# Optimization experiments

Hardware: AMD Instinct MI355X
Metric: run time of the kernel (lower is better)

Reference implementation:

```python
import jax, jax.numpy as jnp
import numpy as np

NUM_DAYOFWEEK, NUM_TIME, NUM_MONTH, NUM_DAY = 7, 24, 12, 31
NUM_DESTINATION = 100000
NUM_FACTOR = 128
NUM_DIM = NUM_FACTOR // 4  # 32
N = 1048576


def setup_inputs() -> dict:
    key = jax.random.key(0)
    ks = jax.random.split(key, 10)
    std = 0.1
    return {
        "dayofweek": jax.random.randint(ks[0], (N,), 0, NUM_DAYOFWEEK),
        "time": jax.random.randint(ks[1], (N,), 0, NUM_TIME),
        "month": jax.random.randint(ks[2], (N,), 0, NUM_MONTH),
        "day": jax.random.randint(ks[3], (N,), 0, NUM_DAY),
        "destination": jax.random.randint(ks[4], (N,), 0, NUM_DESTINATION),
        "W_dayofweek": std * jax.random.normal(ks[5], (NUM_DAYOFWEEK, NUM_DIM), dtype=jnp.float32),
        "W_time": std * jax.random.normal(ks[6], (NUM_TIME, NUM_DIM), dtype=jnp.float32),
        "W_month": std * jax.random.normal(ks[7], (NUM_MONTH, NUM_DIM), dtype=jnp.float32),
        "W_day": std * jax.random.normal(ks[8], (NUM_DAY, NUM_DIM), dtype=jnp.float32),
        "W_item": std * jax.random.normal(ks[9], (NUM_DESTINATION, NUM_FACTOR), dtype=jnp.float32),
    }


def reference(dayofweek, time, month, day, destination,
              W_dayofweek, W_time, W_month, W_day, W_item) -> jnp.ndarray:
    # Gather per-feature embeddings and concat into user vector [N, num_factor]
    user = jnp.concatenate([
        W_dayofweek[dayofweek],  # [N, 32]
        W_time[time],            # [N, 32]
        W_month[month],          # [N, 32]
        W_day[day],              # [N, 32]
    ], axis=-1)
    item = W_item[destination]   # [N, 128]
    # Original: diagonal(mm(user, item.T)) == rowwise dot product; compute it directly.
    return jnp.sum(user * item, axis=-1)  # [N]
```

## Files before the change

### kernel.cpp

```cpp
#include <hip/hip_runtime.h>


constexpr int NDIM = 32;
constexpr int TS   = 36;
constexpr int R_DOW = 7, R_TIM = 24, R_MON = 12, R_DAY = 31;
constexpr int B_DOW = 0;
constexpr int B_TIM = B_DOW + R_DOW * TS;
constexpr int B_MON = B_TIM + R_TIM * TS;
constexpr int B_DAY = B_MON + R_MON * TS;
constexpr int TAB_TOT = B_DAY + R_DAY * TS;

constexpr int NB   = 32;
constexpr int DDIV = 3125;
constexpr int NBLK = 512;
constexpr int SPB  = 2048;
constexpr int IPT  = SPB / 256;

typedef unsigned long long u64;

__device__ __forceinline__ void load_tab(float* tab, const float* Wdow, const float* Wtim,
                                         const float* Wmon, const float* Wday) {
    const int t = threadIdx.x;
    for (int i = t; i < R_DOW * NDIM; i += 256) tab[B_DOW + (i >> 5) * TS + (i & 31)] = Wdow[i];
    for (int i = t; i < R_TIM * NDIM; i += 256) tab[B_TIM + (i >> 5) * TS + (i & 31)] = Wtim[i];
    for (int i = t; i < R_MON * NDIM; i += 256) tab[B_MON + (i >> 5) * TS + (i & 31)] = Wmon[i];
    for (int i = t; i < R_DAY * NDIM; i += 256) tab[B_DAY + (i >> 5) * TS + (i & 31)] = Wday[i];
}

__global__ __launch_bounds__(256, 2)
void bin_kernel(const int* __restrict__ dow, const int* __restrict__ tim,
                const int* __restrict__ mon, const int* __restrict__ day,
                const int* __restrict__ dest,
                int* __restrict__ cntG, int* __restrict__ lbaseG,
                u64* __restrict__ payload, unsigned short* __restrict__ invl, int n)
{
    __shared__ u64 stage[SPB];
    __shared__ unsigned short ist[SPB];
    __shared__ int hist[NB], lbase[NB], cursor[NB];

    const int t = threadIdx.x, b = blockIdx.x;
    const int g0 = b * SPB;
    const int rem = n - g0;
    const int len = rem < SPB ? rem : SPB;

    int dreg[IPT], pkreg[IPT];
#pragma unroll
    for (int i = 0; i < IPT; i++) {
        const int k = i * 256 + t;
        if (k < len) {
            const int idx = g0 + k;
            dreg[i]  = dest[idx];
            pkreg[i] = dow[idx] | (tim[idx] << 3) | (mon[idx] << 8) | (day[idx] << 12);
        } else { dreg[i] = -1; pkreg[i] = 0; }
    }
    if (t < NB) hist[t] = 0;
    __syncthreads();
#pragma unroll
    for (int i = 0; i < IPT; i++)
        if (dreg[i] >= 0) atomicAdd(&hist[dreg[i] / DDIV], 1);
    __syncthreads();
    if (t == 0) {
        int run = 0;
        for (int q = 0; q < NB; q++) { lbase[q] = run; run += hist[q]; }
    }
    __syncthreads();
    if (t < NB) { cursor[t] = lbase[t]; cntG[b * NB + t] = hist[t]; lbaseG[b * NB + t] = lbase[t]; }
    __syncthreads();
#pragma unroll
    for (int i = 0; i < IPT; i++) {
        const int k = i * 256 + t;
        if (k < len) {
            const int ds = dreg[i];
            const int j  = atomicAdd(&cursor[ds / DDIV], 1);
            stage[j] = (u64)(unsigned)(g0 + k)
                     | ((u64)(unsigned)ds       << 20)
                     | ((u64)(unsigned)pkreg[i] << 37);
            ist[k] = (unsigned short)j;
        }
    }
    __syncthreads();
#pragma unroll
    for (int i = 0; i < IPT; i++) {
        const int k = i * 256 + t;
        if (k < len) {
            payload[g0 + k] = stage[k];
            invl[g0 + k]    = ist[k];
        }
    }
}

__global__ __launch_bounds__(256, 8)
void mf_main_kernel(const u64* __restrict__ payload,
                    const float* __restrict__ Wdow, const float* __restrict__ Wtim,
                    const float* __restrict__ Wmon, const float* __restrict__ Wday,
                    const float* __restrict__ Witem,
                    const int* __restrict__ cntG, const int* __restrict__ lbaseG,
                    float* __restrict__ res)
{
    __shared__ float tab[TAB_TOT];
    load_tab(tab, Wdow, Wtim, Wmon, Wday);
    __syncthreads();

    const int tid = threadIdx.x;
    const int sub = tid & 63;
    const int wv  = tid >> 6;
    const int g   = sub >> 3;
    const int l8  = sub & 7;
    const int col = l8 * 4;
    const int tb[4] = {B_DOW, B_TIM, B_MON, B_DAY};
    const int sh[4] = {37, 40, 45, 49};
    const int mk[4] = {7, 31, 15, 31};

    const int x = blockIdx.x & 7;
    const int s = blockIdx.x >> 3;

    for (int p = 0; p < 4; p++) {
        const int q  = x + 8 * p;
        const int L  = cntG[s * NB + q];
        const int st = s * SPB + lbaseG[s * NB + q];

        for (int i = wv * 16; i < L; i += 64) {
            const int i0 = i + g, i1 = i + 8 + g;
            const bool v0 = i0 < L, v1 = i1 < L;

            const u64 p0 = v0 ? payload[st + i0] : 0ull;
            const u64 p1 = v1 ? payload[st + i1] : 0ull;

            const int d0 = (int)((p0 >> 20) & 0x1FFFFull);
            const int d1 = (int)((p1 >> 20) & 0x1FFFFull);

            const float* r0 = Witem + (long)d0 * 128 + col;
            const float* r1 = Witem + (long)d1 * 128 + col;

            float4 it0[4], it1[4], us0[4], us1[4];
#pragma unroll
            for (int j = 0; j < 4; j++) it0[j] = *reinterpret_cast<const float4*>(r0 + j * NDIM);
#pragma unroll
            for (int j = 0; j < 4; j++) it1[j] = *reinterpret_cast<const float4*>(r1 + j * NDIM);
#pragma unroll
            for (int j = 0; j < 4; j++) {
                const int idx = (int)((p0 >> sh[j]) & (u64)mk[j]);
                us0[j] = *reinterpret_cast<const float4*>(&tab[tb[j] + idx * TS + col]);
            }
#pragma unroll
            for (int j = 0; j < 4; j++) {
                const int idx = (int)((p1 >> sh[j]) & (u64)mk[j]);
                us1[j] = *reinterpret_cast<const float4*>(&tab[tb[j] + idx * TS + col]);
            }

            float a0 = 0.f, a1 = 0.f;
#pragma unroll
            for (int j = 0; j < 4; j++) {
                a0 += it0[j].x * us0[j].x + it0[j].y * us0[j].y
                    + it0[j].z * us0[j].z + it0[j].w * us0[j].w;
                a1 += it1[j].x * us1[j].x + it1[j].y * us1[j].y
                    + it1[j].z * us1[j].z + it1[j].w * us1[j].w;
            }

            a0 += __shfl_xor(a0, 1);  a1 += __shfl_xor(a1, 1);
            a0 += __shfl_xor(a0, 2);  a1 += __shfl_xor(a1, 2);
            a0 += __shfl_xor(a0, 4);  a1 += __shfl_xor(a1, 4);

            if (l8 == 0) {
                if (v0) res[st + i0] = a0;
                if (v1) res[st + i1] = a1;
            }
        }
    }
}

__global__ __launch_bounds__(256, 2)
void unperm_kernel(const float* __restrict__ res, const unsigned short* __restrict__ invl,
                   float* __restrict__ out, int n)
{
    __shared__ float r[SPB];
    const int t = threadIdx.x, b = blockIdx.x;
    const int g0 = b * SPB;
    const int rem = n - g0;
    const int len = rem < SPB ? rem : SPB;
#pragma unroll
    for (int i = 0; i < IPT; i++) {
        const int k = i * 256 + t;
        if (k < len) r[k] = res[g0 + k];
    }
    __syncthreads();
#pragma unroll
    for (int i = 0; i < IPT; i++) {
        const int k = i * 256 + t;
        if (k < len) out[g0 + k] = r[invl[g0 + k]];
    }
}

__global__ __launch_bounds__(256, 8)
void mf_dot_kernel(const int* __restrict__ dow, const int* __restrict__ tim,
                   const int* __restrict__ mon, const int* __restrict__ day,
                   const int* __restrict__ dest,
                   const float* __restrict__ Wdow, const float* __restrict__ Wtim,
                   const float* __restrict__ Wmon, const float* __restrict__ Wday,
                   const float* __restrict__ Witem,
                   float* __restrict__ out, int n_samples)
{
    __shared__ float tab[TAB_TOT];
    load_tab(tab, Wdow, Wtim, Wmon, Wday);
    __syncthreads();
    const int tid = threadIdx.x;
    const int lane = tid & 63, sub = lane & 31, wave = tid >> 6, half = lane >> 5;
    const int t = sub >> 3, dofs = (sub & 7) * 4;
    const int* idxp  = (t == 0) ? dow   : (t == 1) ? tim   : (t == 2) ? mon   : day;
    const int  tbase = (t == 0) ? B_DOW : (t == 1) ? B_TIM : (t == 2) ? B_MON : B_DAY;
    long n = (long)blockIdx.x * 8 + wave * 2 + half;
    const long stride = (long)gridDim.x * 8;
    for (; n < n_samples; n += stride) {
        const int idx = idxp[n];
        const int ds  = dest[n];
        const float4 u  = *reinterpret_cast<const float4*>(&tab[tbase + idx * TS + dofs]);
        const float4 it = *reinterpret_cast<const float4*>(&Witem[(long)ds * 128 + sub * 4]);
        float r = u.x * it.x + u.y * it.y + u.z * it.z + u.w * it.w;
        r += __shfl_xor(r, 16); r += __shfl_xor(r, 8); r += __shfl_xor(r, 4);
        r += __shfl_xor(r, 2);  r += __shfl_xor(r, 1);
        if (sub == 0) out[n] = r;
    }
}

extern "C" void kernel_launch(void* const* d_in, const int* in_sizes, int n_in,
                              void* d_out, int out_size, void* d_ws, size_t ws_size,
                              hipStream_t stream)
{
    const int*   dow   = (const int*)d_in[0];
    const int*   tim   = (const int*)d_in[1];
    const int*   mon   = (const int*)d_in[2];
    const int*   day   = (const int*)d_in[3];
    const int*   dest  = (const int*)d_in[4];
    const float* Wdow  = (const float*)d_in[5];
    const float* Wtim  = (const float*)d_in[6];
    const float* Wmon  = (const float*)d_in[7];
    const float* Wday  = (const float*)d_in[8];
    const float* Witem = (const float*)d_in[9];
    float* out = (float*)d_out;

    const int n = in_sizes[0];
    const int cap = NBLK * SPB;

    const size_t off_payload = 128 * 1024;
    const size_t off_invl    = off_payload + (size_t)cap * 8;
    const size_t off_res     = off_invl + (size_t)cap * 2;
    const size_t need        = off_res + (size_t)cap * 4;

    if ((size_t)ws_size < need || n > cap) {
        hipLaunchKernelGGL(mf_dot_kernel, dim3(2048), dim3(256), 0, stream,
                           dow, tim, mon, day, dest,
                           Wdow, Wtim, Wmon, Wday, Witem, out, n);
        return;
    }

    int* cntG    = (int*)d_ws;
    int* lbaseG  = (int*)((char*)d_ws + 64 * 1024);
    u64* payload = (u64*)((char*)d_ws + off_payload);
    unsigned short* invl = (unsigned short*)((char*)d_ws + off_invl);
    float* res           = (float*)((char*)d_ws + off_res);

    hipLaunchKernelGGL(bin_kernel, dim3(NBLK), dim3(256), 0, stream,
                       dow, tim, mon, day, dest, cntG, lbaseG, payload, invl, n);
    hipLaunchKernelGGL(mf_main_kernel, dim3(NBLK * 8), dim3(256), 0, stream,
                       payload, Wdow, Wtim, Wmon, Wday, Witem, cntG, lbaseG, res);
    hipLaunchKernelGGL(unperm_kernel, dim3(NBLK), dim3(256), 0, stream,
                       res, invl, out, n);
}
```

Before: 162.1 us.

## Enlarge bin segments to 4096 samples, drop table padding, hoist bucket metadata

Doubles the per-block segment in the binning and unpermute kernels to 4096 samples using 1024-thread blocks. This halves the segment count, so each destination bucket in the main kernel gets longer runs with better Witem locality and fewer tiny tail iterations. It also removes the 36-float row padding of the shared embedding tables, hoists the per-bucket count and base loads ahead of the main loop, and prefetches the inverse-permutation indices before the barrier in unpermute. In exchange, the main kernel's grid halves to 2048 blocks and the bin kernel uses more shared memory per block. Unpadded rows may also bring back LDS bank conflicts on the float4 table reads.

```diff
diff --git a/kernel.cpp b/kernel.cpp
--- a/kernel.cpp
+++ b/kernel.cpp
@@ -2,32 +2,32 @@
 
 
 constexpr int NDIM = 32;
-constexpr int TS   = 36;
-constexpr int R_DOW = 7, R_TIM = 24, R_MON = 12, R_DAY = 31;
+constexpr int SZ_DOW = 7 * NDIM, SZ_TIM = 24 * NDIM, SZ_MON = 12 * NDIM, SZ_DAY = 31 * NDIM;
 constexpr int B_DOW = 0;
-constexpr int B_TIM = B_DOW + R_DOW * TS;
-constexpr int B_MON = B_TIM + R_TIM * TS;
-constexpr int B_DAY = B_MON + R_MON * TS;
-constexpr int TAB_TOT = B_DAY + R_DAY * TS;
-
-constexpr int NB   = 32;
-constexpr int DDIV = 3125;
-constexpr int NBLK = 512;
-constexpr int SPB  = 2048;
-constexpr int IPT  = SPB / 256;
+constexpr int B_TIM = B_DOW + SZ_DOW;
+constexpr int B_MON = B_TIM + SZ_TIM;
+constexpr int B_DAY = B_MON + SZ_MON;
+constexpr int TAB_TOT = B_DAY + SZ_DAY;
+
+constexpr int NB    = 32;
+constexpr int DDIV  = 3125;
+constexpr int NBLK  = 256;
+constexpr int SPB   = 4096;
+constexpr int BIN_T = 1024;
+constexpr int IPT   = SPB / BIN_T;
 
 typedef unsigned long long u64;
 
 __device__ __forceinline__ void load_tab(float* tab, const float* Wdow, const float* Wtim,
-                                         const float* Wmon, const float* Wday) {
+                                         const float* Wmon, const float* Wday, int nthr) {
     const int t = threadIdx.x;
-    for (int i = t; i < R_DOW * NDIM; i += 256) tab[B_DOW + (i >> 5) * TS + (i & 31)] = Wdow[i];
-    for (int i = t; i < R_TIM * NDIM; i += 256) tab[B_TIM + (i >> 5) * TS + (i & 31)] = Wtim[i];
-    for (int i = t; i < R_MON * NDIM; i += 256) tab[B_MON + (i >> 5) * TS + (i & 31)] = Wmon[i];
-    for (int i = t; i < R_DAY * NDIM; i += 256) tab[B_DAY + (i >> 5) * TS + (i & 31)] = Wday[i];
-}
-
-__global__ __launch_bounds__(256, 2)
+    for (int i = t; i < SZ_DOW; i += nthr) tab[B_DOW + i] = Wdow[i];
+    for (int i = t; i < SZ_TIM; i += nthr) tab[B_TIM + i] = Wtim[i];
+    for (int i = t; i < SZ_MON; i += nthr) tab[B_MON + i] = Wmon[i];
+    for (int i = t; i < SZ_DAY; i += nthr) tab[B_DAY + i] = Wday[i];
+}
+
+__global__ __launch_bounds__(BIN_T)
 void bin_kernel(const int* __restrict__ dow, const int* __restrict__ tim,
                 const int* __restrict__ mon, const int* __restrict__ day,
                 const int* __restrict__ dest,
@@ -46,7 +46,7 @@
     int dreg[IPT], pkreg[IPT];
 #pragma unroll
     for (int i = 0; i < IPT; i++) {
-        const int k = i * 256 + t;
+        const int k = i * BIN_T + t;
         if (k < len) {
             const int idx = g0 + k;
             dreg[i]  = dest[idx];
@@ -68,7 +68,7 @@
     __syncthreads();
 #pragma unroll
     for (int i = 0; i < IPT; i++) {
-        const int k = i * 256 + t;
+        const int k = i * BIN_T + t;
         if (k < len) {
             const int ds = dreg[i];
             const int j  = atomicAdd(&cursor[ds / DDIV], 1);
@@ -81,7 +81,7 @@
     __syncthreads();
 #pragma unroll
     for (int i = 0; i < IPT; i++) {
-        const int k = i * 256 + t;
+        const int k = i * BIN_T + t;
         if (k < len) {
             payload[g0 + k] = stage[k];
             invl[g0 + k]    = ist[k];
@@ -98,7 +98,7 @@
                     float* __restrict__ res)
 {
     __shared__ float tab[TAB_TOT];
-    load_tab(tab, Wdow, Wtim, Wmon, Wday);
+    load_tab(tab, Wdow, Wtim, Wmon, Wday, 256);
     __syncthreads();
 
     const int tid = threadIdx.x;
@@ -114,10 +114,18 @@
     const int x = blockIdx.x & 7;
     const int s = blockIdx.x >> 3;
 
+    int Ls[4], sts[4];
+#pragma unroll
     for (int p = 0; p < 4; p++) {
-        const int q  = x + 8 * p;
-        const int L  = cntG[s * NB + q];
-        const int st = s * SPB + lbaseG[s * NB + q];
+        const int q = x + 8 * p;
+        Ls[p]  = cntG[s * NB + q];
+        sts[p] = s * SPB + lbaseG[s * NB + q];
+    }
+
+#pragma unroll
+    for (int p = 0; p < 4; p++) {
+        const int L  = Ls[p];
+        const int st = sts[p];
 
         for (int i = wv * 16; i < L; i += 64) {
             const int i0 = i + g, i1 = i + 8 + g;
@@ -140,12 +148,12 @@
 #pragma unroll
             for (int j = 0; j < 4; j++) {
                 const int idx = (int)((p0 >> sh[j]) & (u64)mk[j]);
-                us0[j] = *reinterpret_cast<const float4*>(&tab[tb[j] + idx * TS + col]);
+                us0[j] = *reinterpret_cast<const float4*>(&tab[tb[j] + idx * NDIM + col]);
             }
 #pragma unroll
             for (int j = 0; j < 4; j++) {
                 const int idx = (int)((p1 >> sh[j]) & (u64)mk[j]);
-                us1[j] = *reinterpret_cast<const float4*>(&tab[tb[j] + idx * TS + col]);
+                us1[j] = *reinterpret_cast<const float4*>(&tab[tb[j] + idx * NDIM + col]);
             }
 
             float a0 = 0.f, a1 = 0.f;
@@ -169,7 +177,7 @@
     }
 }
 
-__global__ __launch_bounds__(256, 2)
+__global__ __launch_bounds__(BIN_T)
 void unperm_kernel(const float* __restrict__ res, const unsigned short* __restrict__ invl,
                    float* __restrict__ out, int n)
 {
@@ -178,16 +186,19 @@
     const int g0 = b * SPB;
     const int rem = n - g0;
     const int len = rem < SPB ? rem : SPB;
-#pragma unroll
-    for (int i = 0; i < IPT; i++) {
-        const int k = i * 256 + t;
+
+    unsigned short iv[IPT];
+#pragma unroll
+    for (int i = 0; i < IPT; i++) {
+        const int k = i * BIN_T + t;
+        iv[i] = (k < len) ? invl[g0 + k] : 0;
         if (k < len) r[k] = res[g0 + k];
     }
     __syncthreads();
 #pragma unroll
     for (int i = 0; i < IPT; i++) {
-        const int k = i * 256 + t;
-        if (k < len) out[g0 + k] = r[invl[g0 + k]];
+        const int k = i * BIN_T + t;
+        if (k < len) out[g0 + k] = r[iv[i]];
     }
 }
 
@@ -201,7 +212,7 @@
                    float* __restrict__ out, int n_samples)
 {
     __shared__ float tab[TAB_TOT];
-    load_tab(tab, Wdow, Wtim, Wmon, Wday);
+    load_tab(tab, Wdow, Wtim, Wmon, Wday, 256);
     __syncthreads();
     const int tid = threadIdx.x;
     const int lane = tid & 63, sub = lane & 31, wave = tid >> 6, half = lane >> 5;
@@ -213,7 +224,7 @@
     for (; n < n_samples; n += stride) {
         const int idx = idxp[n];
         const int ds  = dest[n];
-        const float4 u  = *reinterpret_cast<const float4*>(&tab[tbase + idx * TS + dofs]);
+        const float4 u  = *reinterpret_cast<const float4*>(&tab[tbase + idx * NDIM + dofs]);
         const float4 it = *reinterpret_cast<const float4*>(&Witem[(long)ds * 128 + sub * 4]);
         float r = u.x * it.x + u.y * it.y + u.z * it.z + u.w * it.w;
         r += __shfl_xor(r, 16); r += __shfl_xor(r, 8); r += __shfl_xor(r, 4);
@@ -241,7 +252,7 @@
     const int n = in_sizes[0];
     const int cap = NBLK * SPB;
 
-    const size_t off_payload = 128 * 1024;
+    const size_t off_payload = 64 * 1024;
     const size_t off_invl    = off_payload + (size_t)cap * 8;
     const size_t off_res     = off_invl + (size_t)cap * 2;
     const size_t need        = off_res + (size_t)cap * 4;
@@ -254,15 +265,15 @@
     }
 
     int* cntG    = (int*)d_ws;
-    int* lbaseG  = (int*)((char*)d_ws + 64 * 1024);
+    int* lbaseG  = (int*)((char*)d_ws + 32 * 1024);
     u64* payload = (u64*)((char*)d_ws + off_payload);
     unsigned short* invl = (unsigned short*)((char*)d_ws + off_invl);
     float* res           = (float*)((char*)d_ws + off_res);
 
-    hipLaunchKernelGGL(bin_kernel, dim3(NBLK), dim3(256), 0, stream,
+    hipLaunchKernelGGL(bin_kernel, dim3(NBLK), dim3(BIN_T), 0, stream,
                        dow, tim, mon, day, dest, cntG, lbaseG, payload, invl, n);
     hipLaunchKernelGGL(mf_main_kernel, dim3(NBLK * 8), dim3(256), 0, stream,
                        payload, Wdow, Wtim, Wmon, Wday, Witem, cntG, lbaseG, res);
-    hipLaunchKernelGGL(unperm_kernel, dim3(NBLK), dim3(256), 0, stream,
+    hipLaunchKernelGGL(unperm_kernel, dim3(NBLK), dim3(BIN_T), 0, stream,
                        res, invl, out, n);
 }
```

Result: faster. 153.9 us (-5.1%).
